# Performance work log

Hardware: AMD Instinct MI355X
Metric: run time of the kernel (lower is better)

Reference implementation:

```python
import jax, jax.numpy as jnp
import numpy as np

N_EMBD = 384
HEAD_SIZE = 16

def setup_inputs() -> dict:
    key = jax.random.key(0)
    k1, k2, k3, k4 = jax.random.split(key, 4)
    B, T = 4, 4096
    x = jax.random.normal(k1, (B, T, N_EMBD), dtype=jnp.float32)
    # nn.Linear(n_embd, head_size, bias=False): y = x @ W^T, W: [head_size, n_embd].
    # Store transposed [n_embd, head_size] for direct matmul.
    s = 1.0 / np.sqrt(N_EMBD)
    Wk = jax.random.uniform(k2, (N_EMBD, HEAD_SIZE), jnp.float32, -s, s)
    Wq = jax.random.uniform(k3, (N_EMBD, HEAD_SIZE), jnp.float32, -s, s)
    Wv = jax.random.uniform(k4, (N_EMBD, HEAD_SIZE), jnp.float32, -s, s)
    return {"x": x, "Wk": Wk, "Wq": Wq, "Wv": Wv}

def reference(x, Wk, Wq, Wv):
    B, T, C = x.shape
    k = x @ Wk  # [B,T,H]
    q = x @ Wq
    v = x @ Wv
    scale = k.shape[-1] ** -0.5
    wei = jnp.einsum('bth,bsh->bts', q, k) * scale  # [B,T,T]
    causal = jnp.tril(jnp.ones((T, T), dtype=bool))
    wei = jnp.where(causal, wei, -jnp.inf)
    wei = jax.nn.softmax(wei, axis=-1)
    out = jnp.einsum('bts,bsh->bth', wei, v)  # [B,T,H]
    return out
```

## Files before the change

### kernel.cpp

```cpp
#include <hip/hip_runtime.h>


constexpr int B_DIM = 4;
constexpr int T_SEQ = 4096;
constexpr int C_DIM = 384;
constexpr int H_DIM = 16;
constexpr int NROW  = B_DIM * T_SEQ;

typedef __bf16 bf16x8 __attribute__((ext_vector_type(8)));
typedef float  f32x4  __attribute__((ext_vector_type(4)));

__device__ __forceinline__ unsigned short f2bf(float f) {
  unsigned int u = __builtin_bit_cast(unsigned int, f);
  u += 0x7fffu + ((u >> 16) & 1u);
  return (unsigned short)(u >> 16);
}
__device__ __forceinline__ bf16x8 as_bf16x8(uint4 u) {
  return __builtin_bit_cast(bf16x8, u);
}
__device__ __forceinline__ unsigned cvt_pk_bf16(float lo, float hi) {
  unsigned r;
  asm("v_cvt_pk_bf16_f32 %0, %1, %2" : "=v"(r) : "v"(lo), "v"(hi));
  return r;
}

__global__ __launch_bounds__(256) void wconv(
    const float* __restrict__ Wk, const float* __restrict__ Wq,
    const float* __restrict__ Wv, unsigned short* __restrict__ WT) {
  const int i = blockIdx.x * 256 + threadIdx.x;
  const int m = i / 6144;
  const int r = i - m * 6144;
  const int n = r / 384;
  const int k = r - n * 384;
  const float* __restrict__ W = (m == 0) ? Wk : (m == 1) ? Wq : Wv;
  WT[i] = f2bf(W[k * 16 + n]);
}

__global__ __launch_bounds__(128) void qkv_mfma(
    const float* __restrict__ x, const unsigned short* __restrict__ WT,
    unsigned short* __restrict__ Kb,
    unsigned short* __restrict__ Qb,
    unsigned short* __restrict__ VTb)
{
  const int tid  = threadIdx.x;
  const int w    = tid >> 6;
  const int lane = tid & 63;
  const int quad = lane >> 4;
  const int col  = lane & 15;
  const int r0   = blockIdx.x << 4;
  const int kb   = w * 6;

  __shared__ float mrg[12][64];

  const float4* __restrict__ xp =
      reinterpret_cast<const float4*>(x + (size_t)(r0 + col) * C_DIM) + quad * 2;
  float4 araw[12];
#pragma unroll
  for (int kk = 0; kk < 6; ++kk) {
    araw[2 * kk]     = xp[(kb + kk) * 8];
    araw[2 * kk + 1] = xp[(kb + kk) * 8 + 1];
  }

  const uint4* __restrict__ bk = reinterpret_cast<const uint4*>(
      WT + (size_t)col * 384 + quad * 8);
  const uint4* __restrict__ bq = bk + 768;
  const uint4* __restrict__ bv = bk + 1536;

  f32x4 ck = {0.f, 0.f, 0.f, 0.f};
  f32x4 cq = {0.f, 0.f, 0.f, 0.f};
  f32x4 cv = {0.f, 0.f, 0.f, 0.f};
#pragma unroll
  for (int kk = 0; kk < 6; ++kk) {
    uint4 pk;
    const float4 a0 = araw[2 * kk], a1 = araw[2 * kk + 1];
    pk.x = cvt_pk_bf16(a0.x, a0.y);
    pk.y = cvt_pk_bf16(a0.z, a0.w);
    pk.z = cvt_pk_bf16(a1.x, a1.y);
    pk.w = cvt_pk_bf16(a1.z, a1.w);
    const bf16x8 av = as_bf16x8(pk);
    ck = __builtin_amdgcn_mfma_f32_16x16x32_bf16(av, as_bf16x8(bk[(kb + kk) * 4]), ck, 0, 0, 0);
    cq = __builtin_amdgcn_mfma_f32_16x16x32_bf16(av, as_bf16x8(bq[(kb + kk) * 4]), cq, 0, 0, 0);
    cv = __builtin_amdgcn_mfma_f32_16x16x32_bf16(av, as_bf16x8(bv[(kb + kk) * 4]), cv, 0, 0, 0);
  }

  if (w == 1) {
#pragma unroll
    for (int r = 0; r < 4; ++r) {
      mrg[r][lane]     = ck[r];
      mrg[4 + r][lane] = cq[r];
      mrg[8 + r][lane] = cv[r];
    }
  }
  __syncthreads();
  if (w == 0) {
    const float SC = 0.25f * 1.44269504088896341f;
#pragma unroll
    for (int r = 0; r < 4; ++r) {
      const float vk = ck[r] + mrg[r][lane];
      const float vq = cq[r] + mrg[4 + r][lane];
      const float vv = cv[r] + mrg[8 + r][lane];
      const int row = r0 + quad * 4 + r;
      Kb[row * 16 + col]      = f2bf(vk);
      Qb[row * 32 + col]      = f2bf(vq * SC);
      Qb[row * 32 + 16 + col] = 0;
      const int bb = row >> 12, t = row & 4095;
      VTb[(((size_t)(bb * 16 + col)) << 12) + t] = f2bf(vv);
    }
  }
}

__global__ __launch_bounds__(512) void flash_v9(
    const unsigned short* __restrict__ Qb,
    const unsigned short* __restrict__ Kb,
    const unsigned short* __restrict__ VTb,
    float* __restrict__ out)
{
  const int tid  = threadIdx.x;
  const int w    = tid >> 6;
  const int lane = tid & 63;
  const int quad = lane >> 4;
  const int col  = lane & 15;
  const int p    = blockIdx.x >> 2;
  const int b    = blockIdx.x & 3;
  const int qtA  = 255 - p;
  const int qtB  = p;
  const int nchA = (qtA + 4) >> 2;

  __shared__ __attribute__((aligned(16))) unsigned short Pl[8][16 * 72];
  __shared__ float mO[8][2][256];
  __shared__ float mL[8][2][16];
  unsigned short* const P = Pl[w];

  const unsigned short* Kbase = Kb + ((size_t)(b * T_SEQ) << 4);
  const unsigned short* Vbase = VTb + (((size_t)(b * 16 + col)) << 12);
  const int poff = col * 72 + quad * 4;

  f32x4 o = {0.f, 0.f, 0.f, 0.f};

  const uint4* qpA = reinterpret_cast<const uint4*>(
      Qb + (((size_t)(b * T_SEQ + (qtA << 4) + col)) << 5) + quad * 8);
  const uint4* qpB = reinterpret_cast<const uint4*>(
      Qb + (((size_t)(b * T_SEQ + (qtB << 4) + col)) << 5) + quad * 8);
  const bf16x8 qaA = as_bf16x8(qpA[0]);
  const bf16x8 qaB = as_bf16x8(qpB[0]);

  auto loadK = [&](int c, uint4* k4) {
    const int kt0 = c << 2;
#pragma unroll
    for (int t = 0; t < 4; ++t)
      k4[t] = *reinterpret_cast<const uint4*>(
          Kbase + (((size_t)((kt0 + t) * 16 + col)) << 4) + quad * 8);
  };
  auto loadV = [&](int c, uint4* v2) {
    v2[0] = *reinterpret_cast<const uint4*>(Vbase + c * 64 + quad * 8);
    v2[1] = *reinterpret_cast<const uint4*>(Vbase + c * 64 + 32 + quad * 8);
  };

  auto computeP = [&](int qt, bf16x8 qa, int c, const uint4* k4, float& lref) {
    const int kt0 = c << 2;
    float lsum = 0.f;
#pragma unroll
    for (int t = 0; t < 4; ++t) {
      const int kt = kt0 + t;
      f32x4 sf;
      if (kt <= qt) {
        f32x4 z = {0.f, 0.f, 0.f, 0.f};
        sf = __builtin_amdgcn_mfma_f32_16x16x32_bf16(as_bf16x8(k4[t]), qa, z, 0, 0, 0);
        if (kt == qt) {
#pragma unroll
          for (int r = 0; r < 4; ++r)
            if (quad * 4 + r > col) sf[r] = -1e30f;
        }
      } else {
#pragma unroll
        for (int r = 0; r < 4; ++r) sf[r] = -1e30f;
      }
      const float p0 = __builtin_amdgcn_exp2f(sf[0]);
      const float p1 = __builtin_amdgcn_exp2f(sf[1]);
      const float p2 = __builtin_amdgcn_exp2f(sf[2]);
      const float p3 = __builtin_amdgcn_exp2f(sf[3]);
      lsum += (p0 + p1) + (p2 + p3);
      uint2 pr;
      pr.x = cvt_pk_bf16(p0, p1);
      pr.y = cvt_pk_bf16(p2, p3);
      *reinterpret_cast<uint2*>(P + poff + t * 16) = pr;
    }
    lref += lsum;
  };

  auto doPV = [&](const uint4* v2) {
    const uint2* pp = reinterpret_cast<const uint2*>(P + col * 72);
    const uint2 a0 = pp[quad * 2],     a1 = pp[quad * 2 + 1];
    const uint2 b0 = pp[8 + quad * 2], b1 = pp[8 + quad * 2 + 1];
    const uint4 p0 = {a0.x, a0.y, a1.x, a1.y};
    const uint4 p1 = {b0.x, b0.y, b1.x, b1.y};
    o = __builtin_amdgcn_mfma_f32_16x16x32_bf16(as_bf16x8(p0), as_bf16x8(v2[0]), o, 0, 0, 0);
    o = __builtin_amdgcn_mfma_f32_16x16x32_bf16(as_bf16x8(p1), as_bf16x8(v2[1]), o, 0, 0, 0);
  };

  auto writePartial = [&](int ph, float lsum) {
    float l = lsum;
    l += __shfl_xor(l, 16);
    l += __shfl_xor(l, 32);
#pragma unroll
    for (int r = 0; r < 4; ++r)
      mO[w][ph][(quad * 4 + r) * 16 + col] = o[r];
    if (quad == 0) mL[w][ph][col] = l;
  };

  float lA = 0.f, lB = 0.f;
  uint4 k4[4], vcur[2], vnxt[2];

  int g = w;
  loadK(g, k4);
  loadV(g, vcur);
  computeP(qtA, qaA, g, k4, lA);

  int prevg = g;
  g += 8;
  while (g < 65) {
    const int c = (g < nchA) ? g : g - nchA;
    loadK(c, k4);
    loadV(c, vnxt);
    doPV(vcur);
    asm volatile("" ::: "memory");
    if (prevg < nchA && g >= nchA) {
      writePartial(0, lA);
      o = (f32x4){0.f, 0.f, 0.f, 0.f};
    }
    if (g < nchA) computeP(qtA, qaA, c, k4, lA);
    else          computeP(qtB, qaB, c, k4, lB);
    vcur[0] = vnxt[0];
    vcur[1] = vnxt[1];
    prevg = g;
    g += 8;
  }
  doPV(vcur);
  if (prevg < nchA) {
    writePartial(0, lA);
    o = (f32x4){0.f, 0.f, 0.f, 0.f};
    writePartial(1, 0.f);
  } else {
    writePartial(1, lB);
  }

  __syncthreads();

  {
    const int ph = tid >> 8;
    const int i  = tid & 255;
    float O = 0.f, L = 0.f;
#pragma unroll
    for (int ww = 0; ww < 8; ++ww) {
      O += mO[ww][ph][i];
      L += mL[ww][ph][i >> 4];
    }
    const int qt = ph ? qtB : qtA;
    out[(size_t)(b * T_SEQ + (qt << 4)) * 16 + i] = O / L;
  }
}

extern "C" void kernel_launch(void* const* d_in, const int* in_sizes, int n_in,
                              void* d_out, int out_size, void* d_ws, size_t ws_size,
                              hipStream_t stream) {
  const float* x  = (const float*)d_in[0];
  const float* Wk = (const float*)d_in[1];
  const float* Wq = (const float*)d_in[2];
  const float* Wv = (const float*)d_in[3];
  float* outp = (float*)d_out;

  unsigned short* Qb  = (unsigned short*)d_ws;
  unsigned short* Kb  = Qb + (size_t)NROW * 32;
  unsigned short* VTb = Kb + (size_t)NROW * 16 + 64;
  unsigned short* WT  = VTb + (size_t)NROW * 16;

  wconv<<<72, 256, 0, stream>>>(Wk, Wq, Wv, WT);
  qkv_mfma<<<1024, 128, 0, stream>>>(x, WT, Kb, Qb, VTb);
  flash_v9<<<512, 512, 0, stream>>>(Qb, Kb, VTb, outp);
}
```

Baseline: 94.82 us.

## Fuse weight conversion into QKV projection kernel via shared-memory transposed weights

Removes the separate wconv launch. Each 512-thread block of the new qkvw kernel converts all three weight matrices to bf16 and stores them transposed in LDS with a padded row stride, then processes four 16-row tiles instead of one. This saves a kernel launch and the global round trip for the transposed weights. In exchange, every block redundantly reads and converts all 18K weights, and each block uses about 37KB of LDS, which may limit occupancy.

```diff
diff --git a/kernel.cpp b/kernel.cpp
--- a/kernel.cpp
+++ b/kernel.cpp
@@ -7,6 +7,9 @@
 constexpr int H_DIM = 16;
 constexpr int NROW  = B_DIM * T_SEQ;
 
+constexpr int WTROW = 392;
+constexpr int WTMAT = 16 * WTROW;
+
 typedef __bf16 bf16x8 __attribute__((ext_vector_type(8)));
 typedef float  f32x4  __attribute__((ext_vector_type(4)));
 
@@ -24,33 +27,40 @@
   return r;
 }
 
-__global__ __launch_bounds__(256) void wconv(
-    const float* __restrict__ Wk, const float* __restrict__ Wq,
-    const float* __restrict__ Wv, unsigned short* __restrict__ WT) {
-  const int i = blockIdx.x * 256 + threadIdx.x;
-  const int m = i / 6144;
-  const int r = i - m * 6144;
-  const int n = r / 384;
-  const int k = r - n * 384;
-  const float* __restrict__ W = (m == 0) ? Wk : (m == 1) ? Wq : Wv;
-  WT[i] = f2bf(W[k * 16 + n]);
-}
-
-__global__ __launch_bounds__(128) void qkv_mfma(
-    const float* __restrict__ x, const unsigned short* __restrict__ WT,
+__global__ __launch_bounds__(512) void qkvw(
+    const float* __restrict__ x,  const float* __restrict__ Wk,
+    const float* __restrict__ Wq, const float* __restrict__ Wv,
     unsigned short* __restrict__ Kb,
     unsigned short* __restrict__ Qb,
     unsigned short* __restrict__ VTb)
 {
+  __shared__ __attribute__((aligned(16))) unsigned short WTl[3 * WTMAT];
+  __shared__ float mrg[4][12 * 64];
+
   const int tid  = threadIdx.x;
   const int w    = tid >> 6;
   const int lane = tid & 63;
   const int quad = lane >> 4;
   const int col  = lane & 15;
-  const int r0   = blockIdx.x << 4;
-  const int kb   = w * 6;
-
-  __shared__ float mrg[12][64];
+  const int pair = w >> 1;
+  const int kw   = w & 1;
+  const int tile = (blockIdx.x << 2) | pair;
+  const int r0   = tile << 4;
+  const int kb   = kw * 6;
+
+  {
+    const float* const Ws[3] = {Wk, Wq, Wv};
+#pragma unroll
+    for (int e = 0; e < 36; ++e) {
+      const int i = e * 512 + tid;
+      const int m = i / 6144;
+      const int r = i - m * 6144;
+      const int n = r / 384;
+      const int k = r - n * 384;
+      WTl[m * WTMAT + n * WTROW + k] = f2bf(Ws[m][k * 16 + n]);
+    }
+  }
+  __syncthreads();
 
   const float4* __restrict__ xp =
       reinterpret_cast<const float4*>(x + (size_t)(r0 + col) * C_DIM) + quad * 2;
@@ -61,10 +71,7 @@
     araw[2 * kk + 1] = xp[(kb + kk) * 8 + 1];
   }
 
-  const uint4* __restrict__ bk = reinterpret_cast<const uint4*>(
-      WT + (size_t)col * 384 + quad * 8);
-  const uint4* __restrict__ bq = bk + 768;
-  const uint4* __restrict__ bv = bk + 1536;
+  const unsigned short* const bkl = WTl + col * WTROW + quad * 8;
 
   f32x4 ck = {0.f, 0.f, 0.f, 0.f};
   f32x4 cq = {0.f, 0.f, 0.f, 0.f};
@@ -78,27 +85,31 @@
     pk.z = cvt_pk_bf16(a1.x, a1.y);
     pk.w = cvt_pk_bf16(a1.z, a1.w);
     const bf16x8 av = as_bf16x8(pk);
-    ck = __builtin_amdgcn_mfma_f32_16x16x32_bf16(av, as_bf16x8(bk[(kb + kk) * 4]), ck, 0, 0, 0);
-    cq = __builtin_amdgcn_mfma_f32_16x16x32_bf16(av, as_bf16x8(bq[(kb + kk) * 4]), cq, 0, 0, 0);
-    cv = __builtin_amdgcn_mfma_f32_16x16x32_bf16(av, as_bf16x8(bv[(kb + kk) * 4]), cv, 0, 0, 0);
-  }
-
-  if (w == 1) {
+    const int ko = (kb + kk) * 32;
+    const uint4 fk = *reinterpret_cast<const uint4*>(bkl + ko);
+    const uint4 fq = *reinterpret_cast<const uint4*>(bkl + WTMAT + ko);
+    const uint4 fv = *reinterpret_cast<const uint4*>(bkl + 2 * WTMAT + ko);
+    ck = __builtin_amdgcn_mfma_f32_16x16x32_bf16(av, as_bf16x8(fk), ck, 0, 0, 0);
+    cq = __builtin_amdgcn_mfma_f32_16x16x32_bf16(av, as_bf16x8(fq), cq, 0, 0, 0);
+    cv = __builtin_amdgcn_mfma_f32_16x16x32_bf16(av, as_bf16x8(fv), cv, 0, 0, 0);
+  }
+
+  if (kw == 1) {
 #pragma unroll
     for (int r = 0; r < 4; ++r) {
-      mrg[r][lane]     = ck[r];
-      mrg[4 + r][lane] = cq[r];
-      mrg[8 + r][lane] = cv[r];
+      mrg[pair][r * 64 + lane]       = ck[r];
+      mrg[pair][(4 + r) * 64 + lane] = cq[r];
+      mrg[pair][(8 + r) * 64 + lane] = cv[r];
     }
   }
   __syncthreads();
-  if (w == 0) {
+  if (kw == 0) {
     const float SC = 0.25f * 1.44269504088896341f;
 #pragma unroll
     for (int r = 0; r < 4; ++r) {
-      const float vk = ck[r] + mrg[r][lane];
-      const float vq = cq[r] + mrg[4 + r][lane];
-      const float vv = cv[r] + mrg[8 + r][lane];
+      const float vk = ck[r] + mrg[pair][r * 64 + lane];
+      const float vq = cq[r] + mrg[pair][(4 + r) * 64 + lane];
+      const float vv = cv[r] + mrg[pair][(8 + r) * 64 + lane];
       const int row = r0 + quad * 4 + r;
       Kb[row * 16 + col]      = f2bf(vk);
       Qb[row * 32 + col]      = f2bf(vq * SC);
@@ -272,9 +283,7 @@
   unsigned short* Qb  = (unsigned short*)d_ws;
   unsigned short* Kb  = Qb + (size_t)NROW * 32;
   unsigned short* VTb = Kb + (size_t)NROW * 16 + 64;
-  unsigned short* WT  = VTb + (size_t)NROW * 16;
-
-  wconv<<<72, 256, 0, stream>>>(Wk, Wq, Wv, WT);
-  qkv_mfma<<<1024, 128, 0, stream>>>(x, WT, Kb, Qb, VTb);
+
+  qkvw<<<256, 512, 0, stream>>>(x, Wk, Wq, Wv, Kb, Qb, VTb);
   flash_v9<<<512, 512, 0, stream>>>(Qb, Kb, VTb, outp);
 }
```

Result: slower. 98.42 us (+3.8%).
